# Optimization experiments

Hardware: AMD Instinct MI355X
Metric: run time of the kernel (lower is better)

## Reference

```python
import jax, jax.numpy as jnp
import numpy as np

N = 100000
E = 3200000
NODE_IN = 118
D = 32
H = 4
C = D // H  # 8
EDGE_DIM = 50 + 3
L = 4
LN_EPS = 1e-5


def _layernorm(x, g, b):
    mu = jnp.mean(x, axis=-1, keepdims=True)
    var = jnp.mean(jnp.square(x - mu), axis=-1, keepdims=True)
    return (x - mu) * jax.lax.rsqrt(var + LN_EPS) * g + b


def setup_inputs() -> dict:
    key = jax.random.key(0)
    ks = jax.random.split(key, 20)
    x = jax.random.normal(ks[0], (N, NODE_IN), dtype=jnp.float32)
    edge_index = jax.random.randint(ks[1], (2, E), 0, N, dtype=jnp.int32)
    edge_len = jax.random.normal(ks[2], (E, 50), dtype=jnp.float32)
    edge_vec = jax.random.normal(ks[3], (E, 3), dtype=jnp.float32)
    s_in = 1.0 / np.sqrt(NODE_IN)
    s_d = 1.0 / np.sqrt(D)
    s_e = 1.0 / np.sqrt(EDGE_DIM)
    node_in_W = jax.random.normal(ks[4], (NODE_IN, D), dtype=jnp.float32) * s_in
    node_in_b = jnp.zeros((D,), dtype=jnp.float32)
    ln_g = jnp.ones((L, D), dtype=jnp.float32)
    ln_b = jnp.zeros((L, D), dtype=jnp.float32)
    Wq = jax.random.normal(ks[5], (L, D, D), dtype=jnp.float32) * s_d
    bq = jnp.zeros((L, D), dtype=jnp.float32)
    Wk = jax.random.normal(ks[6], (L, D, D), dtype=jnp.float32) * s_d
    bk = jnp.zeros((L, D), dtype=jnp.float32)
    Wv = jax.random.normal(ks[7], (L, D, D), dtype=jnp.float32) * s_d
    bv = jnp.zeros((L, D), dtype=jnp.float32)
    We = jax.random.normal(ks[8], (L, EDGE_DIM, D), dtype=jnp.float32) * s_e  # lin_edge, bias=False
    Wskip = jax.random.normal(ks[9], (L, D, D), dtype=jnp.float32) * s_d
    bskip = jnp.zeros((L, D), dtype=jnp.float32)
    return {"x": x, "edge_index": edge_index, "edge_len": edge_len, "edge_vec": edge_vec,
            "node_in_W": node_in_W, "node_in_b": node_in_b, "ln_g": ln_g, "ln_b": ln_b,
            "Wq": Wq, "bq": bq, "Wk": Wk, "bk": bk, "Wv": Wv, "bv": bv,
            "We": We, "Wskip": Wskip, "bskip": bskip}


def reference(x, edge_index, edge_len, edge_vec, node_in_W, node_in_b, ln_g, ln_b,
              Wq, bq, Wk, bk, Wv, bv, We, Wskip, bskip):
    src = edge_index[0]  # j (source), messages flow source -> target
    dst = edge_index[1]  # i (target), softmax grouped by dst
    ef = jnp.concatenate([edge_len, edge_vec], axis=-1)  # [E, 53]
    h = x @ node_in_W + node_in_b  # [N, D]
    scale = 1.0 / np.sqrt(C)
    for l in range(L):
        xn = _layernorm(h, ln_g[l], ln_b[l])
        q = (xn @ Wq[l] + bq[l]).reshape(N, H, C)
        k = (xn @ Wk[l] + bk[l]).reshape(N, H, C)
        v = (xn @ Wv[l] + bv[l]).reshape(N, H, C)
        e = (ef @ We[l]).reshape(E, H, C)  # per-edge key/value shift
        kj = k[src] + e                     # [E, H, C]
        alpha = jnp.sum(q[dst] * kj, axis=-1) * scale  # [E, H]
        # segment softmax over incoming edges of each target node
        amax = jax.ops.segment_max(alpha, dst, num_segments=N)  # [N, H]
        amax = jnp.where(jnp.isfinite(amax), amax, 0.0)
        ex = jnp.exp(alpha - amax[dst])
        denom = jax.ops.segment_sum(ex, dst, num_segments=N)
        w = ex / (denom[dst] + 1e-16)       # [E, H]
        msg = (v[src] + e) * w[:, :, None]  # [E, H, C]
        agg = jax.ops.segment_sum(msg.reshape(E, H * C), dst, num_segments=N)  # [N, D]
        y = agg + xn @ Wskip[l] + bskip[l]  # concat heads + root skip (lin_skip(x_i))
        h = h + y                            # residual
    return h
```

## Files before the change

### kernel.cpp

```cpp
#include <hip/hip_runtime.h>
#include <hip/hip_bf16.h>
#include <math.h>

#define N_NODES 100000
#define N_EDGES 3200000
#define NODE_IN 118
#define DIM 32
#define EDF 53
#define NLAYER 4

typedef __attribute__((ext_vector_type(8))) short short8;
typedef __attribute__((ext_vector_type(4))) short short4v;
typedef __attribute__((ext_vector_type(4))) float f32x4;
typedef unsigned short u16;
typedef unsigned int u32;

static __device__ __forceinline__ float bfhi2f(u32 hi) {
    union { u32 i; float f; } x; x.i = hi; return x.f;
}
static __device__ __forceinline__ u16 f2bf(float f) {
    union { float f; u32 i; } x; x.f = f;
    u32 i = x.i;
    return (u16)((i + 0x7FFFu + ((i >> 16) & 1u)) >> 16);
}

__global__ __launch_bounds__(256) void k_count(const int* __restrict__ dst, int* __restrict__ cnt) {
    int e = blockIdx.x * 256 + threadIdx.x;
    atomicAdd(&cnt[dst[e]], 1);
}

__global__ __launch_bounds__(256) void k_scanA(const int* __restrict__ cnt, int* __restrict__ off,
                                               int* __restrict__ bsum) {
    __shared__ int s[256];
    int t = threadIdx.x; int i = blockIdx.x * 256 + t;
    int v = (i < N_NODES) ? cnt[i] : 0;
    s[t] = v; __syncthreads();
    for (int d = 1; d < 256; d <<= 1) {
        int x = (t >= d) ? s[t - d] : 0; __syncthreads();
        s[t] += x; __syncthreads();
    }
    if (i < N_NODES) off[i] = s[t] - v;
    if (t == 255) bsum[blockIdx.x] = s[t];
}

__global__ __launch_bounds__(512) void k_scanB(int* bsum, int nb) {
    __shared__ int s[512];
    int t = threadIdx.x;
    int v = (t < nb) ? bsum[t] : 0;
    s[t] = v; __syncthreads();
    for (int d = 1; d < 512; d <<= 1) {
        int x = (t >= d) ? s[t - d] : 0; __syncthreads();
        s[t] += x; __syncthreads();
    }
    if (t < nb) bsum[t] = s[t] - v;
}

__global__ __launch_bounds__(256) void k_scanC(int* off, const int* __restrict__ bsum) {
    int i = blockIdx.x * 256 + threadIdx.x;
    if (i < N_NODES) off[i] += bsum[blockIdx.x];
    if (i == 0) off[N_NODES] = N_EDGES;
}

__global__ __launch_bounds__(256) void k_fill(const int* __restrict__ src, const int* __restrict__ dst,
                                              const int* __restrict__ off, int* __restrict__ cur,
                                              int* __restrict__ eidx, int* __restrict__ esrc) {
    int e = blockIdx.x * 256 + threadIdx.x;
    int d = dst[e];
    int p = off[d] + atomicAdd(&cur[d], 1);
    eidx[p] = e;
    esrc[p] = src[e];
}

__global__ __launch_bounds__(256) void k_init(const float* __restrict__ x, const float* __restrict__ W,
                                              const float* __restrict__ b, float* __restrict__ h) {
    __shared__ float Ws[NODE_IN * DIM];
    __shared__ float xs[8][NODE_IN];
    int t = threadIdx.x;
    for (int i = t; i < NODE_IN * DIM; i += 256) Ws[i] = W[i];
    int nb = blockIdx.x * 8;
    for (int i = t; i < 8 * NODE_IN; i += 256) {
        int n = i / NODE_IN, j = i % NODE_IN;
        xs[n][j] = x[(size_t)(nb + n) * NODE_IN + j];
    }
    __syncthreads();
    int n = t >> 5, c = t & 31;
    float acc = b[c];
    #pragma unroll 2
    for (int j = 0; j < NODE_IN; j++) acc += xs[n][j] * Ws[j * DIM + c];
    h[(size_t)(nb + n) * DIM + c] = acc;
}

template <int NL>
__global__ __launch_bounds__(256) void k_egemm(const float* __restrict__ elen, const float* __restrict__ evec,
                                               const float* __restrict__ We, u16* __restrict__ eout) {
    int tid = threadIdx.x;
    int lane = tid & 63;
    int wv = (blockIdx.x * 256 + tid) >> 6;
    int nw = (gridDim.x * 256) >> 6;
    int n15 = lane & 15, kb = lane >> 4;

    short8 bf[2][2 * NL];
    for (int s = 0; s < 2; s++) {
        for (int t = 0; t < 2 * NL; t++) {
            int n = t * 16 + n15;
            int lay = n >> 5, c = n & 31;
            short8 tmp;
            #pragma unroll
            for (int j = 0; j < 8; j++) {
                int kk = s * 32 + kb * 8 + j;
                float w = (kk < EDF) ? We[(size_t)lay * EDF * DIM + (size_t)kk * DIM + c] : 0.f;
                ((u16*)&tmp)[j] = f2bf(w);
            }
            bf[s][t] = tmp;
        }
    }

    const int NT = N_EDGES / 16;

    auto LOADA = [&](int tile, float* fv) {
        int pos = tile * 16 + n15;
        const float* lp = elen + (size_t)pos * 50;
        {
            const float2* p2 = (const float2*)(lp + kb * 8);
            #pragma unroll
            for (int j = 0; j < 4; j++) { float2 t2 = p2[j]; fv[2 * j] = t2.x; fv[2 * j + 1] = t2.y; }
        }
        if (kb < 2) {
            const float2* p2 = (const float2*)(lp + 32 + kb * 8);
            #pragma unroll
            for (int j = 0; j < 4; j++) { float2 t2 = p2[j]; fv[8 + 2 * j] = t2.x; fv[8 + 2 * j + 1] = t2.y; }
        } else if (kb == 2) {
            float2 t2 = *(const float2*)(lp + 48);
            const float* vp = evec + (size_t)pos * 3;
            fv[8] = t2.x; fv[9] = t2.y; fv[10] = vp[0]; fv[11] = vp[1]; fv[12] = vp[2];
            fv[13] = 0.f; fv[14] = 0.f; fv[15] = 0.f;
        } else {
            #pragma unroll
            for (int j = 8; j < 16; j++) fv[j] = 0.f;
        }
    };

    float cur[16];
    if (wv < NT) LOADA(wv, cur);

    for (int tile = wv; tile < NT; tile += nw) {
        int nxt = tile + nw;
        float nx[16];
        if (nxt < NT) LOADA(nxt, nx);

        short8 af[2];
        #pragma unroll
        for (int s = 0; s < 2; s++) {
            short8 tmp;
            #pragma unroll
            for (int j = 0; j < 8; j++) ((u16*)&tmp)[j] = f2bf(cur[s * 8 + j]);
            af[s] = tmp;
        }

        size_t rowbase = ((size_t)tile * 16 + n15) * DIM;
        #pragma unroll
        for (int t = 0; t < 2 * NL; t++) {
            f32x4 z = {0.f, 0.f, 0.f, 0.f};
            z = __builtin_amdgcn_mfma_f32_16x16x32_bf16(bf[0][t], af[0], z, 0, 0, 0);
            z = __builtin_amdgcn_mfma_f32_16x16x32_bf16(bf[1][t], af[1], z, 0, 0, 0);
            int lay = t >> 1;
            int ch = (t & 1) * 16 + kb * 4;
            short4v sv;
            #pragma unroll
            for (int r = 0; r < 4; r++) ((u16*)&sv)[r] = f2bf(z[r]);
            *(short4v*)&eout[(size_t)lay * N_EDGES * DIM + rowbase + ch] = sv;
        }

        #pragma unroll
        for (int j = 0; j < 16; j++) cur[j] = nx[j];
    }
}

__global__ __launch_bounds__(256) void k_node(const float* __restrict__ h,
        const float* __restrict__ g, const float* __restrict__ bta,
        const float* __restrict__ Wq, const float* __restrict__ bq,
        const float* __restrict__ Wk, const float* __restrict__ bk,
        const float* __restrict__ Wv, const float* __restrict__ bv,
        const float* __restrict__ Ws, const float* __restrict__ bs,
        float* __restrict__ qo, u16* __restrict__ ko, u16* __restrict__ vo, float* __restrict__ hso) {
    __shared__ float WQ[DIM * DIM], WK[DIM * DIM], WV[DIM * DIM], WS[DIM * DIM];
    __shared__ float xn[8][DIM];
    int t = threadIdx.x;
    for (int i = t; i < DIM * DIM; i += 256) { WQ[i] = Wq[i]; WK[i] = Wk[i]; WV[i] = Wv[i]; WS[i] = Ws[i]; }
    int n = t >> 5, c = t & 31;
    size_t node = (size_t)blockIdx.x * 8 + n;
    float hv = h[node * DIM + c];
    float s1 = hv;
    for (int d = 1; d < 32; d <<= 1) s1 += __shfl_xor(s1, d, 64);
    float mu = s1 * (1.f / 32.f);
    float dv = hv - mu;
    float s2 = dv * dv;
    for (int d = 1; d < 32; d <<= 1) s2 += __shfl_xor(s2, d, 64);
    float inv = rsqrtf(s2 * (1.f / 32.f) + 1e-5f);
    float xv = dv * inv * g[c] + bta[c];
    xn[n][c] = xv;
    __syncthreads();
    float aq = bq[c], ak = bk[c], av = bv[c], as = bs[c];
    #pragma unroll 4
    for (int j = 0; j < DIM; j++) {
        float xj = xn[n][j];
        aq += xj * WQ[j * DIM + c];
        ak += xj * WK[j * DIM + c];
        av += xj * WV[j * DIM + c];
        as += xj * WS[j * DIM + c];
    }
    size_t o = node * DIM + c;
    qo[o] = aq * 0.35355339059327373f;
    ko[o] = f2bf(ak);
    vo[o] = f2bf(av);
    hso[o] = hv + as;
}

__global__ __launch_bounds__(256) void k_aggr(const int* __restrict__ off, const int* __restrict__ eidx,
        const int* __restrict__ esrc, const u16* __restrict__ eb,
        const float* __restrict__ qb, const u16* __restrict__ kb, const u16* __restrict__ vb,
        const float* __restrict__ hs, float* __restrict__ out) {
    int tid = threadIdx.x;
    size_t node = (size_t)blockIdx.x * 4 + (tid >> 6);
    int lane = tid & 63;
    int eg = lane >> 3, cq = lane & 7, c0 = cq * 4;
    float4 qv = *(const float4*)&qb[node * DIM + c0];
    int o0 = off[node], o1 = off[node + 1];
    float4 nacc = {0.f, 0.f, 0.f, 0.f};
    float dacc = 0.f;

    int pA = o0 + eg;  bool aA = pA < o1; int qAi = aA ? pA : o0;
    int eA = eidx[qAi], sA = esrc[qAi];
    int pB = pA + 8;   bool aB = pB < o1; int qBi = aB ? pB : o0;
    int eB = eidx[qBi], sB = esrc[qBi];
    int pC = pB + 8;   bool aC = pC < o1; int qCi = aC ? pC : o0;
    int eC = eidx[qCi], sC = esrc[qCi];

    uint2 dAe = *(const uint2*)&eb[(size_t)eA * DIM + c0];
    uint2 dAk = *(const uint2*)&kb[(size_t)sA * DIM + c0];
    uint2 dAv = *(const uint2*)&vb[(size_t)sA * DIM + c0];
    uint2 dBe = *(const uint2*)&eb[(size_t)eB * DIM + c0];
    uint2 dBk = *(const uint2*)&kb[(size_t)sB * DIM + c0];
    uint2 dBv = *(const uint2*)&vb[(size_t)sB * DIM + c0];

    for (int p = o0; p < o1; p += 8) {
        uint2 dCe = *(const uint2*)&eb[(size_t)eC * DIM + c0];
        uint2 dCk = *(const uint2*)&kb[(size_t)sC * DIM + c0];
        uint2 dCv = *(const uint2*)&vb[(size_t)sC * DIM + c0];
        int pD = pC + 8; bool aD = pD < o1; int qDi = aD ? pD : o0;
        int eD = eidx[qDi], sD = esrc[qDi];

        float e0 = bfhi2f(dAe.x << 16), e1 = bfhi2f(dAe.x & 0xFFFF0000u);
        float e2 = bfhi2f(dAe.y << 16), e3 = bfhi2f(dAe.y & 0xFFFF0000u);
        float k0 = bfhi2f(dAk.x << 16), k1 = bfhi2f(dAk.x & 0xFFFF0000u);
        float k2 = bfhi2f(dAk.y << 16), k3 = bfhi2f(dAk.y & 0xFFFF0000u);
        float v0 = bfhi2f(dAv.x << 16), v1 = bfhi2f(dAv.x & 0xFFFF0000u);
        float v2 = bfhi2f(dAv.y << 16), v3 = bfhi2f(dAv.y & 0xFFFF0000u);
        float a = qv.x * (k0 + e0);
        a = fmaf(qv.y, k1 + e1, a);
        a = fmaf(qv.z, k2 + e2, a);
        a = fmaf(qv.w, k3 + e3, a);
        a += __shfl_xor(a, 1);
        float ex = aA ? __expf(a) : 0.f;
        nacc.x = fmaf(ex, v0 + e0, nacc.x);
        nacc.y = fmaf(ex, v1 + e1, nacc.y);
        nacc.z = fmaf(ex, v2 + e2, nacc.z);
        nacc.w = fmaf(ex, v3 + e3, nacc.w);
        dacc += ex;

        aA = aB; dAe = dBe; dAk = dBk; dAv = dBv;
        aB = aC; dBe = dCe; dBk = dCk; dBv = dCv;
        aC = aD; eC = eD; sC = sD; pC = pD;
    }
    #pragma unroll
    for (int d = 8; d < 64; d <<= 1) {
        nacc.x += __shfl_xor(nacc.x, d);
        nacc.y += __shfl_xor(nacc.y, d);
        nacc.z += __shfl_xor(nacc.z, d);
        nacc.w += __shfl_xor(nacc.w, d);
        dacc   += __shfl_xor(dacc, d);
    }
    if (eg == 0) {
        float inv = 1.f / (dacc + 1e-16f);
        float4 hv = *(const float4*)&hs[node * DIM + c0];
        float4 o;
        o.x = hv.x + nacc.x * inv;
        o.y = hv.y + nacc.y * inv;
        o.z = hv.z + nacc.z * inv;
        o.w = hv.w + nacc.w * inv;
        *(float4*)&out[node * DIM + c0] = o;
    }
}

extern "C" void kernel_launch(void* const* d_in, const int* in_sizes, int n_in,
                              void* d_out, int out_size, void* d_ws, size_t ws_size,
                              hipStream_t stream) {
    const float* x    = (const float*)d_in[0];
    const int*   ei   = (const int*)d_in[1];
    const int*   src  = ei;
    const int*   dst  = ei + N_EDGES;
    const float* elen = (const float*)d_in[2];
    const float* evec = (const float*)d_in[3];
    const float* niW  = (const float*)d_in[4];
    const float* nib  = (const float*)d_in[5];
    const float* lng  = (const float*)d_in[6];
    const float* lnb  = (const float*)d_in[7];
    const float* Wq   = (const float*)d_in[8];
    const float* bq   = (const float*)d_in[9];
    const float* Wk   = (const float*)d_in[10];
    const float* bk   = (const float*)d_in[11];
    const float* Wv   = (const float*)d_in[12];
    const float* bv   = (const float*)d_in[13];
    const float* We   = (const float*)d_in[14];
    const float* Wsk  = (const float*)d_in[15];
    const float* bsk  = (const float*)d_in[16];
    float* out = (float*)d_out;

    unsigned char* w = (unsigned char*)d_ws;
    auto alloc = [&](size_t bytes) -> void* {
        void* p = (void*)w; w += (bytes + 255) & ~(size_t)255; return p;
    };
    int*   off  = (int*)alloc((N_NODES + 1) * sizeof(int));
    int*   cnt  = (int*)alloc(N_NODES * sizeof(int));
    int*   bsum = (int*)alloc(512 * sizeof(int));
    int*   eidx = (int*)alloc((size_t)N_EDGES * sizeof(int));
    int*   esrc = (int*)alloc((size_t)N_EDGES * sizeof(int));
    float* h    = (float*)alloc((size_t)N_NODES * DIM * sizeof(float));
    float* qb   = (float*)alloc((size_t)N_NODES * DIM * sizeof(float));
    u16*   kb   = (u16*)alloc((size_t)N_NODES * DIM * sizeof(u16));
    u16*   vb   = (u16*)alloc((size_t)N_NODES * DIM * sizeof(u16));
    float* hsb  = (float*)alloc((size_t)N_NODES * DIM * sizeof(float));
    size_t used = (size_t)(w - (unsigned char*)d_ws);
    size_t e_full = (size_t)NLAYER * N_EDGES * DIM * sizeof(u16);
    size_t e_one  = (size_t)N_EDGES * DIM * sizeof(u16);
    bool full = (used + e_full) <= ws_size;
    u16* ebuf = (u16*)alloc(full ? e_full : e_one);

    const int EB = N_EDGES / 256;
    const int NB = N_NODES / 8;
    const int AB = N_NODES / 4;
    const int nbScan = (N_NODES + 255) / 256;

    hipMemsetAsync(cnt, 0, N_NODES * sizeof(int), stream);
    k_count<<<EB, 256, 0, stream>>>(dst, cnt);
    k_scanA<<<nbScan, 256, 0, stream>>>(cnt, off, bsum);
    k_scanB<<<1, 512, 0, stream>>>(bsum, nbScan);
    k_scanC<<<nbScan, 256, 0, stream>>>(off, bsum);
    hipMemsetAsync(cnt, 0, N_NODES * sizeof(int), stream);
    k_fill<<<EB, 256, 0, stream>>>(src, dst, off, cnt, eidx, esrc);

    k_init<<<NB, 256, 0, stream>>>(x, niW, nib, h);

    if (full) k_egemm<4><<<4096, 256, 0, stream>>>(elen, evec, We, ebuf);

    for (int l = 0; l < NLAYER; l++) {
        if (!full) k_egemm<1><<<4096, 256, 0, stream>>>(elen, evec, We + (size_t)l * EDF * DIM, ebuf);
        k_node<<<NB, 256, 0, stream>>>(h, lng + l * DIM, lnb + l * DIM,
                                       Wq + (size_t)l * DIM * DIM, bq + l * DIM,
                                       Wk + (size_t)l * DIM * DIM, bk + l * DIM,
                                       Wv + (size_t)l * DIM * DIM, bv + l * DIM,
                                       Wsk + (size_t)l * DIM * DIM, bsk + l * DIM,
                                       qb, kb, vb, hsb);
        const u16* el = full ? (ebuf + (size_t)l * N_EDGES * DIM) : ebuf;
        k_aggr<<<AB, 256, 0, stream>>>(off, eidx, esrc, el, qb, kb, vb, hsb,
                                       (l == NLAYER - 1) ? out : h);
    }
}
```

Before: 1.574 ms.

## Pack edge index pairs, interleave K/V rows, widen per-lane head loads in aggregation

The CSR fill now writes (edge id, source) as one int2, and the node kernel writes K and V side by side in a single 64-wide bf16 row. The aggregation kernel changes its lane mapping so each lane owns a full 8-channel head, using 16-byte loads and removing the cross-lane shuffle for the attention dot product. Sixteen edges are processed per step instead of eight. The edge GEMM uses the packed v_cvt_pk_bf16_f32 conversion instead of manual rounding, which adds per-lane register pressure and may change rounding behaviour slightly.

```diff
diff --git a/kernel.cpp b/kernel.cpp
--- a/kernel.cpp
+++ b/kernel.cpp
@@ -10,7 +10,6 @@
 #define NLAYER 4
 
 typedef __attribute__((ext_vector_type(8))) short short8;
-typedef __attribute__((ext_vector_type(4))) short short4v;
 typedef __attribute__((ext_vector_type(4))) float f32x4;
 typedef unsigned short u16;
 typedef unsigned int u32;
@@ -22,6 +21,11 @@
     union { float f; u32 i; } x; x.f = f;
     u32 i = x.i;
     return (u16)((i + 0x7FFFu + ((i >> 16) & 1u)) >> 16);
+}
+static __device__ __forceinline__ u32 pk2bf(float a, float b) {
+    u32 r;
+    asm("v_cvt_pk_bf16_f32 %0, %1, %2" : "=v"(r) : "v"(a), "v"(b));
+    return r;
 }
 
 __global__ __launch_bounds__(256) void k_count(const int* __restrict__ dst, int* __restrict__ cnt) {
@@ -63,12 +67,11 @@
 
 __global__ __launch_bounds__(256) void k_fill(const int* __restrict__ src, const int* __restrict__ dst,
                                               const int* __restrict__ off, int* __restrict__ cur,
-                                              int* __restrict__ eidx, int* __restrict__ esrc) {
+                                              int2* __restrict__ epk) {
     int e = blockIdx.x * 256 + threadIdx.x;
     int d = dst[e];
     int p = off[d] + atomicAdd(&cur[d], 1);
-    eidx[p] = e;
-    esrc[p] = src[e];
+    epk[p] = make_int2(e, src[e]);
 }
 
 __global__ __launch_bounds__(256) void k_init(const float* __restrict__ x, const float* __restrict__ W,
@@ -148,27 +151,22 @@
         float nx[16];
         if (nxt < NT) LOADA(nxt, nx);
 
-        short8 af[2];
-        #pragma unroll
-        for (int s = 0; s < 2; s++) {
-            short8 tmp;
-            #pragma unroll
-            for (int j = 0; j < 8; j++) ((u16*)&tmp)[j] = f2bf(cur[s * 8 + j]);
-            af[s] = tmp;
-        }
+        union { short8 s; u32 u[4]; } A0, A1;
+        A0.u[0] = pk2bf(cur[0], cur[1]);  A0.u[1] = pk2bf(cur[2], cur[3]);
+        A0.u[2] = pk2bf(cur[4], cur[5]);  A0.u[3] = pk2bf(cur[6], cur[7]);
+        A1.u[0] = pk2bf(cur[8], cur[9]);  A1.u[1] = pk2bf(cur[10], cur[11]);
+        A1.u[2] = pk2bf(cur[12], cur[13]); A1.u[3] = pk2bf(cur[14], cur[15]);
 
         size_t rowbase = ((size_t)tile * 16 + n15) * DIM;
         #pragma unroll
         for (int t = 0; t < 2 * NL; t++) {
             f32x4 z = {0.f, 0.f, 0.f, 0.f};
-            z = __builtin_amdgcn_mfma_f32_16x16x32_bf16(bf[0][t], af[0], z, 0, 0, 0);
-            z = __builtin_amdgcn_mfma_f32_16x16x32_bf16(bf[1][t], af[1], z, 0, 0, 0);
+            z = __builtin_amdgcn_mfma_f32_16x16x32_bf16(bf[0][t], A0.s, z, 0, 0, 0);
+            z = __builtin_amdgcn_mfma_f32_16x16x32_bf16(bf[1][t], A1.s, z, 0, 0, 0);
             int lay = t >> 1;
             int ch = (t & 1) * 16 + kb * 4;
-            short4v sv;
-            #pragma unroll
-            for (int r = 0; r < 4; r++) ((u16*)&sv)[r] = f2bf(z[r]);
-            *(short4v*)&eout[(size_t)lay * N_EDGES * DIM + rowbase + ch] = sv;
+            uint2 sv = { pk2bf(z[0], z[1]), pk2bf(z[2], z[3]) };
+            *(uint2*)&eout[(size_t)lay * N_EDGES * DIM + rowbase + ch] = sv;
         }
 
         #pragma unroll
@@ -182,7 +180,7 @@
         const float* __restrict__ Wk, const float* __restrict__ bk,
         const float* __restrict__ Wv, const float* __restrict__ bv,
         const float* __restrict__ Ws, const float* __restrict__ bs,
-        float* __restrict__ qo, u16* __restrict__ ko, u16* __restrict__ vo, float* __restrict__ hso) {
+        float* __restrict__ qo, u16* __restrict__ kvo, float* __restrict__ hso) {
     __shared__ float WQ[DIM * DIM], WK[DIM * DIM], WV[DIM * DIM], WS[DIM * DIM];
     __shared__ float xn[8][DIM];
     int t = threadIdx.x;
@@ -211,84 +209,89 @@
     }
     size_t o = node * DIM + c;
     qo[o] = aq * 0.35355339059327373f;
-    ko[o] = f2bf(ak);
-    vo[o] = f2bf(av);
+    kvo[node * 64 + c]      = f2bf(ak);
+    kvo[node * 64 + 32 + c] = f2bf(av);
     hso[o] = hv + as;
 }
 
-__global__ __launch_bounds__(256) void k_aggr(const int* __restrict__ off, const int* __restrict__ eidx,
-        const int* __restrict__ esrc, const u16* __restrict__ eb,
-        const float* __restrict__ qb, const u16* __restrict__ kb, const u16* __restrict__ vb,
+__global__ __launch_bounds__(256) void k_aggr(const int* __restrict__ off, const int2* __restrict__ epk,
+        const u16* __restrict__ eb, const float* __restrict__ qb, const u16* __restrict__ kvb,
         const float* __restrict__ hs, float* __restrict__ out) {
     int tid = threadIdx.x;
     size_t node = (size_t)blockIdx.x * 4 + (tid >> 6);
     int lane = tid & 63;
-    int eg = lane >> 3, cq = lane & 7, c0 = cq * 4;
-    float4 qv = *(const float4*)&qb[node * DIM + c0];
+    int eg = lane >> 2, hq = lane & 3, c0 = hq * 8;
+    float4 q0 = *(const float4*)&qb[node * DIM + c0];
+    float4 q1 = *(const float4*)&qb[node * DIM + c0 + 4];
     int o0 = off[node], o1 = off[node + 1];
-    float4 nacc = {0.f, 0.f, 0.f, 0.f};
+    int safe = (o0 < N_EDGES) ? o0 : (N_EDGES - 1);
+    float n0=0.f,n1=0.f,n2=0.f,n3=0.f,n4=0.f,n5=0.f,n6=0.f,n7=0.f;
     float dacc = 0.f;
 
-    int pA = o0 + eg;  bool aA = pA < o1; int qAi = aA ? pA : o0;
-    int eA = eidx[qAi], sA = esrc[qAi];
-    int pB = pA + 8;   bool aB = pB < o1; int qBi = aB ? pB : o0;
-    int eB = eidx[qBi], sB = esrc[qBi];
-    int pC = pB + 8;   bool aC = pC < o1; int qCi = aC ? pC : o0;
-    int eC = eidx[qCi], sC = esrc[qCi];
-
-    uint2 dAe = *(const uint2*)&eb[(size_t)eA * DIM + c0];
-    uint2 dAk = *(const uint2*)&kb[(size_t)sA * DIM + c0];
-    uint2 dAv = *(const uint2*)&vb[(size_t)sA * DIM + c0];
-    uint2 dBe = *(const uint2*)&eb[(size_t)eB * DIM + c0];
-    uint2 dBk = *(const uint2*)&kb[(size_t)sB * DIM + c0];
-    uint2 dBv = *(const uint2*)&vb[(size_t)sB * DIM + c0];
-
-    for (int p = o0; p < o1; p += 8) {
-        uint2 dCe = *(const uint2*)&eb[(size_t)eC * DIM + c0];
-        uint2 dCk = *(const uint2*)&kb[(size_t)sC * DIM + c0];
-        uint2 dCv = *(const uint2*)&vb[(size_t)sC * DIM + c0];
-        int pD = pC + 8; bool aD = pD < o1; int qDi = aD ? pD : o0;
-        int eD = eidx[qDi], sD = esrc[qDi];
+    int pA = o0 + eg;  bool aA = pA < o1; int2 xA = epk[aA ? pA : safe];
+    int pB = pA + 16;  bool aB = pB < o1; int2 xB = epk[aB ? pB : safe];
+    int pC = pB + 16;  bool aC = pC < o1; int2 xC = epk[aC ? pC : safe];
+
+    uint4 dAe = *(const uint4*)&eb[(size_t)xA.x * DIM + c0];
+    uint4 dAk = *(const uint4*)&kvb[(size_t)xA.y * 64 + c0];
+    uint4 dAv = *(const uint4*)&kvb[(size_t)xA.y * 64 + 32 + c0];
+    uint4 dBe = *(const uint4*)&eb[(size_t)xB.x * DIM + c0];
+    uint4 dBk = *(const uint4*)&kvb[(size_t)xB.y * 64 + c0];
+    uint4 dBv = *(const uint4*)&kvb[(size_t)xB.y * 64 + 32 + c0];
+
+    for (int p = o0; p < o1; p += 16) {
+        uint4 dCe = *(const uint4*)&eb[(size_t)xC.x * DIM + c0];
+        uint4 dCk = *(const uint4*)&kvb[(size_t)xC.y * 64 + c0];
+        uint4 dCv = *(const uint4*)&kvb[(size_t)xC.y * 64 + 32 + c0];
+        int pD = pC + 16; bool aD = pD < o1; int2 xD = epk[aD ? pD : safe];
 
         float e0 = bfhi2f(dAe.x << 16), e1 = bfhi2f(dAe.x & 0xFFFF0000u);
         float e2 = bfhi2f(dAe.y << 16), e3 = bfhi2f(dAe.y & 0xFFFF0000u);
+        float e4 = bfhi2f(dAe.z << 16), e5 = bfhi2f(dAe.z & 0xFFFF0000u);
+        float e6 = bfhi2f(dAe.w << 16), e7 = bfhi2f(dAe.w & 0xFFFF0000u);
         float k0 = bfhi2f(dAk.x << 16), k1 = bfhi2f(dAk.x & 0xFFFF0000u);
         float k2 = bfhi2f(dAk.y << 16), k3 = bfhi2f(dAk.y & 0xFFFF0000u);
+        float k4 = bfhi2f(dAk.z << 16), k5 = bfhi2f(dAk.z & 0xFFFF0000u);
+        float k6 = bfhi2f(dAk.w << 16), k7 = bfhi2f(dAk.w & 0xFFFF0000u);
         float v0 = bfhi2f(dAv.x << 16), v1 = bfhi2f(dAv.x & 0xFFFF0000u);
         float v2 = bfhi2f(dAv.y << 16), v3 = bfhi2f(dAv.y & 0xFFFF0000u);
-        float a = qv.x * (k0 + e0);
-        a = fmaf(qv.y, k1 + e1, a);
-        a = fmaf(qv.z, k2 + e2, a);
-        a = fmaf(qv.w, k3 + e3, a);
-        a += __shfl_xor(a, 1);
+        float v4 = bfhi2f(dAv.z << 16), v5 = bfhi2f(dAv.z & 0xFFFF0000u);
+        float v6 = bfhi2f(dAv.w << 16), v7 = bfhi2f(dAv.w & 0xFFFF0000u);
+        float a =      q0.x * (k0 + e0);
+        a = fmaf(q0.y, k1 + e1, a);
+        a = fmaf(q0.z, k2 + e2, a);
+        a = fmaf(q0.w, k3 + e3, a);
+        a = fmaf(q1.x, k4 + e4, a);
+        a = fmaf(q1.y, k5 + e5, a);
+        a = fmaf(q1.z, k6 + e6, a);
+        a = fmaf(q1.w, k7 + e7, a);
         float ex = aA ? __expf(a) : 0.f;
-        nacc.x = fmaf(ex, v0 + e0, nacc.x);
-        nacc.y = fmaf(ex, v1 + e1, nacc.y);
-        nacc.z = fmaf(ex, v2 + e2, nacc.z);
-        nacc.w = fmaf(ex, v3 + e3, nacc.w);
+        n0 = fmaf(ex, v0 + e0, n0); n1 = fmaf(ex, v1 + e1, n1);
+        n2 = fmaf(ex, v2 + e2, n2); n3 = fmaf(ex, v3 + e3, n3);
+        n4 = fmaf(ex, v4 + e4, n4); n5 = fmaf(ex, v5 + e5, n5);
+        n6 = fmaf(ex, v6 + e6, n6); n7 = fmaf(ex, v7 + e7, n7);
         dacc += ex;
 
         aA = aB; dAe = dBe; dAk = dBk; dAv = dBv;
-        aB = aC; dBe = dCe; dBk = dCk; dBv = dCv;
-        aC = aD; eC = eD; sC = sD; pC = pD;
+        dBe = dCe; dBk = dCk; dBv = dCv;
+        aB = aC; xC = xD; aC = aD; pC = pD;
     }
     #pragma unroll
-    for (int d = 8; d < 64; d <<= 1) {
-        nacc.x += __shfl_xor(nacc.x, d);
-        nacc.y += __shfl_xor(nacc.y, d);
-        nacc.z += __shfl_xor(nacc.z, d);
-        nacc.w += __shfl_xor(nacc.w, d);
-        dacc   += __shfl_xor(dacc, d);
+    for (int d = 4; d < 64; d <<= 1) {
+        n0 += __shfl_xor(n0, d); n1 += __shfl_xor(n1, d);
+        n2 += __shfl_xor(n2, d); n3 += __shfl_xor(n3, d);
+        n4 += __shfl_xor(n4, d); n5 += __shfl_xor(n5, d);
+        n6 += __shfl_xor(n6, d); n7 += __shfl_xor(n7, d);
+        dacc += __shfl_xor(dacc, d);
     }
     if (eg == 0) {
         float inv = 1.f / (dacc + 1e-16f);
-        float4 hv = *(const float4*)&hs[node * DIM + c0];
-        float4 o;
-        o.x = hv.x + nacc.x * inv;
-        o.y = hv.y + nacc.y * inv;
-        o.z = hv.z + nacc.z * inv;
-        o.w = hv.w + nacc.w * inv;
-        *(float4*)&out[node * DIM + c0] = o;
+        float4 h0 = *(const float4*)&hs[node * DIM + c0];
+        float4 h1 = *(const float4*)&hs[node * DIM + c0 + 4];
+        float4 o0v = { h0.x + n0 * inv, h0.y + n1 * inv, h0.z + n2 * inv, h0.w + n3 * inv };
+        float4 o1v = { h1.x + n4 * inv, h1.y + n5 * inv, h1.z + n6 * inv, h1.w + n7 * inv };
+        *(float4*)&out[node * DIM + c0] = o0v;
+        *(float4*)&out[node * DIM + c0 + 4] = o1v;
     }
 }
 
@@ -323,12 +326,10 @@
     int*   off  = (int*)alloc((N_NODES + 1) * sizeof(int));
     int*   cnt  = (int*)alloc(N_NODES * sizeof(int));
     int*   bsum = (int*)alloc(512 * sizeof(int));
-    int*   eidx = (int*)alloc((size_t)N_EDGES * sizeof(int));
-    int*   esrc = (int*)alloc((size_t)N_EDGES * sizeof(int));
+    int2*  epk  = (int2*)alloc((size_t)N_EDGES * sizeof(int2));
     float* h    = (float*)alloc((size_t)N_NODES * DIM * sizeof(float));
     float* qb   = (float*)alloc((size_t)N_NODES * DIM * sizeof(float));
-    u16*   kb   = (u16*)alloc((size_t)N_NODES * DIM * sizeof(u16));
-    u16*   vb   = (u16*)alloc((size_t)N_NODES * DIM * sizeof(u16));
+    u16*   kvb  = (u16*)alloc((size_t)N_NODES * 64 * sizeof(u16));
     float* hsb  = (float*)alloc((size_t)N_NODES * DIM * sizeof(float));
     size_t used = (size_t)(w - (unsigned char*)d_ws);
     size_t e_full = (size_t)NLAYER * N_EDGES * DIM * sizeof(u16);
@@ -347,7 +348,7 @@
     k_scanB<<<1, 512, 0, stream>>>(bsum, nbScan);
     k_scanC<<<nbScan, 256, 0, stream>>>(off, bsum);
     hipMemsetAsync(cnt, 0, N_NODES * sizeof(int), stream);
-    k_fill<<<EB, 256, 0, stream>>>(src, dst, off, cnt, eidx, esrc);
+    k_fill<<<EB, 256, 0, stream>>>(src, dst, off, cnt, epk);
 
     k_init<<<NB, 256, 0, stream>>>(x, niW, nib, h);
 
@@ -360,9 +361,9 @@
                                        Wk + (size_t)l * DIM * DIM, bk + l * DIM,
                                        Wv + (size_t)l * DIM * DIM, bv + l * DIM,
                                        Wsk + (size_t)l * DIM * DIM, bsk + l * DIM,
-                                       qb, kb, vb, hsb);
+                                       qb, kvb, hsb);
         const u16* el = full ? (ebuf + (size_t)l * N_EDGES * DIM) : ebuf;
-        k_aggr<<<AB, 256, 0, stream>>>(off, eidx, esrc, el, qb, kb, vb, hsb,
+        k_aggr<<<AB, 256, 0, stream>>>(off, epk, el, qb, kvb, hsb,
                                        (l == NLAYER - 1) ? out : h);
     }
 }
```

New measurement: 1.309 ms. 1.2x faster.
